# Optimization experiments

Measured on AMD Instinct MI355X. Metric: run time of the kernel, lower is better.

## Reference

```python
import jax, jax.numpy as jnp
import numpy as np

DIM = 2048
N_HEADS = 32
N_KV_HEADS = 8
HEAD_DIM = DIM // N_HEADS  # 64
SEQ = 2048
BATCH = 2


def _rope_freqs(seq_len, head_dim, theta=10000.0):
    inv = 1.0 / (theta ** (np.arange(0, head_dim, 2)[: head_dim // 2].astype(np.float32) / head_dim))
    t = np.arange(seq_len, dtype=np.float32)
    ang = np.outer(t, inv)  # (seq, head_dim//2)
    return jnp.asarray(np.cos(ang)), jnp.asarray(np.sin(ang))


def setup_inputs() -> dict:
    key = jax.random.key(0)
    ks = jax.random.split(key, 5)
    x = jax.random.normal(ks[0], (BATCH, SEQ, DIM), dtype=jnp.float32)
    s = 1.0 / np.sqrt(DIM)
    wq = jax.random.normal(ks[1], (N_HEADS * HEAD_DIM, DIM), dtype=jnp.float32) * s
    wk = jax.random.normal(ks[2], (N_KV_HEADS * HEAD_DIM, DIM), dtype=jnp.float32) * s
    wv = jax.random.normal(ks[3], (N_KV_HEADS * HEAD_DIM, DIM), dtype=jnp.float32) * s
    wo = jax.random.normal(ks[4], (DIM, N_HEADS * HEAD_DIM), dtype=jnp.float32) * s
    freqs_cos, freqs_sin = _rope_freqs(SEQ, HEAD_DIM)
    return {"x": x, "freqs_cos": freqs_cos, "freqs_sin": freqs_sin,
            "wq": wq, "wk": wk, "wv": wv, "wo": wo}


def _apply_rope(t, cos, sin):
    # t: (B, S, H, D); cos/sin: (S, D//2) broadcast to (1, S, 1, D//2)
    B, S, H, D = t.shape
    tr = t.reshape(B, S, H, D // 2, 2)
    x0, x1 = tr[..., 0], tr[..., 1]
    c = cos[None, :, None, :]
    s = sin[None, :, None, :]
    o0 = x0 * c - x1 * s
    o1 = x0 * s + x1 * c
    return jnp.stack([o0, o1], axis=-1).reshape(B, S, H, D)


def reference(x, freqs_cos, freqs_sin, wq, wk, wv, wo):
    B, S, _ = x.shape
    H, KV, D = N_HEADS, N_KV_HEADS, HEAD_DIM
    rep = H // KV
    xq = jnp.einsum('bsd,hd->bsh', x, wq).reshape(B, S, H, D)
    xk = jnp.einsum('bsd,hd->bsh', x, wk).reshape(B, S, KV, D)
    xv = jnp.einsum('bsd,hd->bsh', x, wv).reshape(B, S, KV, D)
    xq = _apply_rope(xq, freqs_cos, freqs_sin)
    xk = _apply_rope(xk, freqs_cos, freqs_sin)
    # GQA without materializing repeated K/V: group q heads as (KV, rep).
    # repeat_interleave on dim=2 maps q head h -> kv head h // rep.
    xqg = xq.reshape(B, S, KV, rep, D)
    scale = 1.0 / jnp.sqrt(jnp.float32(D))
    scores = jnp.einsum('bqkrd,bskd->bkrqs', xqg, xk) * scale  # (B,KV,rep,S,S)
    causal = jnp.tril(jnp.ones((S, S), dtype=bool))
    scores = jnp.where(causal[None, None, None], scores, jnp.float32(-jnp.inf))
    probs = jax.nn.softmax(scores, axis=-1)
    out = jnp.einsum('bkrqs,bskd->bqkrd', probs, xv)  # (B,S,KV,rep,D)
    out = out.reshape(B, S, H * D)
    return jnp.einsum('bsh,dh->bsd', out, wo)
```

## Files before the change

kernel.cpp:

```cpp
#include <hip/hip_runtime.h>

#define DIMSZ 2048
#define NH 32
#define NKV 8
#define HD 64
#define SEQLEN 2048
#define BATCH 2
#define NROWS (BATCH*SEQLEN)
#define NQKVC 3072

typedef __bf16 bf16x8 __attribute__((ext_vector_type(8)));
typedef __bf16 bf16x2 __attribute__((ext_vector_type(2)));
typedef float f32x4v __attribute__((ext_vector_type(4)));
typedef float f32x2v __attribute__((ext_vector_type(2)));
typedef float f32x16 __attribute__((ext_vector_type(16)));

__device__ __forceinline__ unsigned short f2bf(float f) {
  __bf16 h = (__bf16)f;
  union { __bf16 h; unsigned short u; } v; v.h = h; return v.u;
}
__device__ __forceinline__ unsigned int pk2bf(float lo, float hi) {
  f32x2v v; v[0] = lo; v[1] = hi;
  bf16x2 h = __builtin_convertvector(v, bf16x2);
  union { bf16x2 h; unsigned int u; } c; c.h = h; return c.u;
}
__device__ __forceinline__ int swz128(int row, int colBytes) {
  return row * 128 + (colBytes ^ ((row & 7) << 4));
}

#define GLOAD16(g, l) __builtin_amdgcn_global_load_lds( \
    (const __attribute__((address_space(1))) unsigned int*)(g), \
    (__attribute__((address_space(3))) unsigned int*)(l), 16, 0, 0)

__global__ void k_cvt_all(const float* __restrict__ x,
                          const float* __restrict__ wq, const float* __restrict__ wk,
                          const float* __restrict__ wv, const float* __restrict__ wo,
                          unsigned short* __restrict__ xb,
                          unsigned short* __restrict__ wqkvb,
                          unsigned short* __restrict__ wob) {
  int i = blockIdx.x * 256 + threadIdx.x;
  const float* s; unsigned short* d; int soff, doff;
  if (i < 2097152)        { s = x;  d = xb;    soff = i;           doff = i; }
  else if (i < 3145728)   { s = wq; d = wqkvb; soff = i - 2097152; doff = i - 2097152; }
  else if (i < 3407872)   { s = wk; d = wqkvb; soff = i - 3145728; doff = i - 2097152; }
  else if (i < 3670016)   { s = wv; d = wqkvb; soff = i - 3407872; doff = i - 2097152; }
  else                    { s = wo; d = wob;   soff = i - 3670016; doff = i - 3670016; }
  float4 v = reinterpret_cast<const float4*>(s)[soff];
  uint2 pk; pk.x = pk2bf(v.x, v.y); pk.y = pk2bf(v.z, v.w);
  reinterpret_cast<uint2*>(d)[doff] = pk;
}

__global__ __launch_bounds__(256, 2) void k_gemm_qkv(
    const unsigned short* __restrict__ A,
    const unsigned short* __restrict__ B,
    const float* __restrict__ fc, const float* __restrict__ fs,
    unsigned short* __restrict__ Qb, unsigned short* __restrict__ Kb,
    unsigned short* __restrict__ Vt)
{
  constexpr int BK = 64, K = DIMSZ;
  __shared__ __attribute__((aligned(16))) unsigned short smA[128 * BK];
  __shared__ __attribute__((aligned(16))) unsigned short smB[128 * BK];
  const int tid = threadIdx.x;
  const int lane = tid & 63;
  const int wid = tid >> 6;
  const int lr = lane & 15, lg = lane >> 4;
  const int gx = gridDim.x;
  int lin = blockIdx.y * gx + blockIdx.x;
  const int cpx = (gx * gridDim.y) >> 3;
  lin = (lin & 7) * cpx + (lin >> 3);
  const int m0 = (lin / gx) * 128, n0 = (lin % gx) * 128;
  const int wr = (wid >> 1) * 64, wc = (wid & 1) * 64;

  f32x4v acc[4][4];
  #pragma unroll
  for (int i = 0; i < 4; i++)
    #pragma unroll
    for (int j = 0; j < 4; j++)
      acc[i][j] = f32x4v{0.f, 0.f, 0.f, 0.f};

  for (int k0 = 0; k0 < K; k0 += BK) {
    #pragma unroll
    for (int c = 0; c < 4; c++) {
      const int chunk = wid * 4 + c;
      const int idx = chunk * 64 + lane;
      const int row = idx >> 3, s = idx & 7;
      const int ks = (s ^ (row & 7)) * 8;
      GLOAD16(A + (size_t)(m0 + row) * K + k0 + ks, &smA[chunk * 512]);
      GLOAD16(B + (size_t)(n0 + row) * K + k0 + ks, &smB[chunk * 512]);
    }
    __syncthreads();
    #pragma unroll
    for (int ks = 0; ks < 2; ks++) {
      bf16x8 af[4], bfv[4];
      #pragma unroll
      for (int m = 0; m < 4; m++)
        af[m] = *reinterpret_cast<const bf16x8*>((char*)smA + swz128(wr + m * 16 + lr, ks * 64 + lg * 16));
      #pragma unroll
      for (int n = 0; n < 4; n++)
        bfv[n] = *reinterpret_cast<const bf16x8*>((char*)smB + swz128(wc + n * 16 + lr, ks * 64 + lg * 16));
      #pragma unroll
      for (int m = 0; m < 4; m++)
        #pragma unroll
        for (int n = 0; n < 4; n++)
          acc[m][n] = __builtin_amdgcn_mfma_f32_16x16x32_bf16(af[m], bfv[n], acc[m][n], 0, 0, 0);
    }
    __syncthreads();
  }
  const int bx = n0 >> 7;
  if (bx < 20) {
    const bool isQ = bx < 16;
    const float SCL = isQ ? 0.18033688011112043f : 1.0f;
    #pragma unroll
    for (int n = 0; n < 4; n++) {
      const int col = n0 + wc + n * 16 + lr;
      const int d = col & 63;
      const int i = d >> 1;
      const float sgn = (d & 1) ? 1.0f : -1.0f;
      unsigned short* dst;
      if (isQ) dst = Qb + (size_t)(col >> 6) * (SEQLEN * HD) + d;
      else     dst = Kb + (size_t)((col - 2048) >> 6) * (SEQLEN * HD) + d;
      #pragma unroll
      for (int m = 0; m < 4; m++)
        #pragma unroll
        for (int r = 0; r < 4; r++) {
          const int row = m0 + wr + m * 16 + lg * 4 + r;
          const int s = row & (SEQLEN - 1), b = row >> 11;
          const float v = acc[m][n][r];
          const float p = __shfl_xor(v, 1);
          const float c = fc[s * 32 + i], sn = fs[s * 32 + i];
          const float o = (v * c + sgn * p * sn) * SCL;
          const size_t headStride = (size_t)(isQ ? NH : NKV) * SEQLEN * HD;
          dst[(size_t)b * headStride + (size_t)s * HD] = f2bf(o);
        }
    }
  } else {
    #pragma unroll
    for (int n = 0; n < 4; n++) {
      const int col = n0 + wc + n * 16 + lr;
      const int kvh = (col - 2560) >> 6, d = col & 63;
      #pragma unroll
      for (int m = 0; m < 4; m++) {
        const int row0 = m0 + wr + m * 16 + lg * 4;
        const int s0 = row0 & (SEQLEN - 1), b = row0 >> 11;
        uint2 pk;
        pk.x = pk2bf(acc[m][n][0], acc[m][n][1]);
        pk.y = pk2bf(acc[m][n][2], acc[m][n][3]);
        *reinterpret_cast<uint2*>(
            Vt + ((size_t)((b * NKV + kvh) * HD) + d) * SEQLEN + s0) = pk;
      }
    }
  }
}

template<int OUT_BF16>
__global__ __launch_bounds__(256, 2) void k_gemm_bt(
    const unsigned short* __restrict__ A,
    const unsigned short* __restrict__ B,
    void* __restrict__ Cv, int M, int N, int K)
{
  constexpr int BK = 64;
  __shared__ __attribute__((aligned(16))) unsigned short smA[128 * BK];
  __shared__ __attribute__((aligned(16))) unsigned short smB[128 * BK];
  const int tid = threadIdx.x;
  const int lane = tid & 63;
  const int wid = tid >> 6;
  const int lr = lane & 15, lg = lane >> 4;
  const int gx = gridDim.x;
  int lin = blockIdx.y * gx + blockIdx.x;
  const int cpx = (gx * gridDim.y) >> 3;
  lin = (lin & 7) * cpx + (lin >> 3);
  const int m0 = (lin / gx) * 128, n0 = (lin % gx) * 128;
  const int wr = (wid >> 1) * 64, wc = (wid & 1) * 64;

  f32x4v acc[4][4];
  #pragma unroll
  for (int i = 0; i < 4; i++)
    #pragma unroll
    for (int j = 0; j < 4; j++)
      acc[i][j] = f32x4v{0.f, 0.f, 0.f, 0.f};

  for (int k0 = 0; k0 < K; k0 += BK) {
    #pragma unroll
    for (int c = 0; c < 4; c++) {
      const int chunk = wid * 4 + c;
      const int idx = chunk * 64 + lane;
      const int row = idx >> 3, s = idx & 7;
      const int ks = (s ^ (row & 7)) * 8;
      GLOAD16(A + (size_t)(m0 + row) * K + k0 + ks, &smA[chunk * 512]);
      GLOAD16(B + (size_t)(n0 + row) * K + k0 + ks, &smB[chunk * 512]);
    }
    __syncthreads();
    #pragma unroll
    for (int ks = 0; ks < 2; ks++) {
      bf16x8 af[4], bfv[4];
      #pragma unroll
      for (int m = 0; m < 4; m++)
        af[m] = *reinterpret_cast<const bf16x8*>((char*)smA + swz128(wr + m * 16 + lr, ks * 64 + lg * 16));
      #pragma unroll
      for (int n = 0; n < 4; n++)
        bfv[n] = *reinterpret_cast<const bf16x8*>((char*)smB + swz128(wc + n * 16 + lr, ks * 64 + lg * 16));
      #pragma unroll
      for (int m = 0; m < 4; m++)
        #pragma unroll
        for (int n = 0; n < 4; n++)
          acc[m][n] = __builtin_amdgcn_mfma_f32_16x16x32_bf16(af[m], bfv[n], acc[m][n], 0, 0, 0);
    }
    __syncthreads();
  }
  #pragma unroll
  for (int m = 0; m < 4; m++)
    #pragma unroll
    for (int n = 0; n < 4; n++)
      #pragma unroll
      for (int r = 0; r < 4; r++) {
        const size_t row = m0 + wr + m * 16 + lg * 4 + r;
        const size_t col = n0 + wc + n * 16 + lr;
        if (OUT_BF16) ((unsigned short*)Cv)[row * N + col] = f2bf(acc[m][n][r]);
        else          ((float*)Cv)[row * N + col] = acc[m][n][r];
      }
}

__global__ __launch_bounds__(256, 2) void k_attn(
    const unsigned short* __restrict__ Qg,
    const unsigned short* __restrict__ Kg,
    const unsigned short* __restrict__ Vt,
    unsigned short* __restrict__ Og)
{
  constexpr int KVB = 64;
  __shared__ __attribute__((aligned(16))) unsigned short sK0[KVB * HD];
  __shared__ __attribute__((aligned(16))) unsigned short sK1[KVB * HD];
  __shared__ __attribute__((aligned(16))) unsigned short sV0[HD * KVB];
  __shared__ __attribute__((aligned(16))) unsigned short sV1[HD * KVB];
  const int tid = threadIdx.x;
  const int lane = tid & 63, wid = tid >> 6;
  const int l31 = lane & 31, hi = lane >> 5;
  const int orig = blockIdx.x;
  const int w = (orig & 7) * 64 + (orig >> 3);
  const int kvh = w >> 6;
  const int b = (w >> 5) & 1;
  const int h = kvh * 4 + ((w >> 3) & 3);
  const int qp = w & 7;
  const unsigned short* Qp = Qg + ((size_t)(b * NH + h) * SEQLEN) * HD;
  const unsigned short* Kp = Kg + ((size_t)(b * NKV + kvh) * SEQLEN) * HD;
  const unsigned short* Vp = Vt + ((size_t)(b * NKV + kvh) * HD) * SEQLEN;

  int srow[2], scol[2];
  #pragma unroll
  for (int cc = 0; cc < 2; cc++) {
    const int idx = (wid * 2 + cc) * 64 + lane;
    srow[cc] = idx >> 3;
    scol[cc] = ((idx & 7) ^ (srow[cc] & 7)) * 8;
  }

  for (int phase = 0; phase < 2; phase++) {
    const int qt = phase ? (15 - qp) : qp;
    const int qrow0 = qt * 128 + wid * 32;
    const int qg = qrow0 + l31;
    bf16x8 aq[4];
    #pragma unroll
    for (int ks = 0; ks < 4; ks++)
      aq[ks] = *reinterpret_cast<const bf16x8*>(Qp + (size_t)qg * HD + ks * 16 + hi * 8);

    f32x16 accO0, accO1;
    #pragma unroll
    for (int ii = 0; ii < 16; ii++) { accO0[ii] = 0.f; accO1[ii] = 0.f; }
    float mrun = -3.0e38f, lrun = 0.f;

    auto STAGE_K = [&](int t, unsigned short* buf) {
      #pragma unroll
      for (int cc = 0; cc < 2; cc++)
        GLOAD16(Kp + (size_t)(t * KVB + srow[cc]) * HD + scol[cc], &buf[(wid * 2 + cc) * 512]);
    };
    auto STAGE_V = [&](int t, unsigned short* buf) {
      #pragma unroll
      for (int cc = 0; cc < 2; cc++)
        GLOAD16(Vp + (size_t)srow[cc] * SEQLEN + t * KVB + scol[cc], &buf[(wid * 2 + cc) * 512]);
    };
    auto QK = [&](int kv0, const unsigned short* bK, f32x16& S0, f32x16& S1) {
      if (kv0 > qrow0 + 31) return;
      #pragma unroll
      for (int ii = 0; ii < 16; ii++) { S0[ii] = 0.f; S1[ii] = 0.f; }
      __builtin_amdgcn_s_setprio(1);
      #pragma unroll
      for (int ks = 0; ks < 4; ks++) {
        bf16x8 ak0 = *reinterpret_cast<const bf16x8*>((const char*)bK + swz128(l31,      ks * 32 + hi * 16));
        bf16x8 ak1 = *reinterpret_cast<const bf16x8*>((const char*)bK + swz128(32 + l31, ks * 32 + hi * 16));
        S0 = __builtin_amdgcn_mfma_f32_32x32x16_bf16(ak0, aq[ks], S0, 0, 0, 0);
        S1 = __builtin_amdgcn_mfma_f32_32x32x16_bf16(ak1, aq[ks], S1, 0, 0, 0);
      }
      __builtin_amdgcn_s_setprio(0);
    };
    auto SMPV = [&](int kv0, const unsigned short* bV, f32x16& S0, f32x16& S1) {
      if (kv0 > qrow0 + 31) return;
      if (kv0 + KVB - 1 > qrow0) {
        #pragma unroll
        for (int reg = 0; reg < 16; reg++) {
          const int rl = (reg & 3) + 8 * (reg >> 2) + (hi << 2);
          if (kv0 + rl > qg)      S0[reg] = -1.0e30f;
          if (kv0 + 32 + rl > qg) S1[reg] = -1.0e30f;
        }
      }
      float t16[16];
      #pragma unroll
      for (int ii = 0; ii < 16; ii++) t16[ii] = fmaxf(S0[ii], S1[ii]);
      float t8[8];
      #pragma unroll
      for (int ii = 0; ii < 8; ii++) t8[ii] = fmaxf(t16[ii], t16[ii + 8]);
      float t4[4];
      #pragma unroll
      for (int ii = 0; ii < 4; ii++) t4[ii] = fmaxf(t8[ii], t8[ii + 4]);
      float tm = fmaxf(fmaxf(t4[0], t4[1]), fmaxf(t4[2], t4[3]));
      tm = fmaxf(tm, __shfl_xor(tm, 32));
      const float mo = mrun;
      const bool defer = __all(tm <= mo + 8.0f);
      const float mn = defer ? mo : fmaxf(mo, tm);
      #pragma unroll
      for (int ii = 0; ii < 16; ii++) {
        S0[ii] = __builtin_amdgcn_exp2f(S0[ii] - mn);
        S1[ii] = __builtin_amdgcn_exp2f(S1[ii] - mn);
      }
      float u16[16];
      #pragma unroll
      for (int ii = 0; ii < 16; ii++) u16[ii] = S0[ii] + S1[ii];
      float u8[8];
      #pragma unroll
      for (int ii = 0; ii < 8; ii++) u8[ii] = u16[ii] + u16[ii + 8];
      float u4[4];
      #pragma unroll
      for (int ii = 0; ii < 4; ii++) u4[ii] = u8[ii] + u8[ii + 4];
      float rs = (u4[0] + u4[1]) + (u4[2] + u4[3]);
      rs += __shfl_xor(rs, 32);
      if (defer) {
        lrun += rs;
      } else {
        const float sc = __builtin_amdgcn_exp2f(mo - mn);
        mrun = mn;
        lrun = lrun * sc + rs;
        #pragma unroll
        for (int reg = 0; reg < 16; reg++) {
          const int rl = (reg & 3) + 8 * (reg >> 2) + (hi << 2);
          const float scr = __shfl(sc, rl);
          accO0[reg] *= scr; accO1[reg] *= scr;
        }
      }
      __builtin_amdgcn_s_setprio(1);
      #define PVSTEP(S16, G, CB) do {                                          \
        unsigned a0 = pk2bf(S16[(G)+0], S16[(G)+1]);                           \
        unsigned a1 = pk2bf(S16[(G)+2], S16[(G)+3]);                           \
        unsigned b0 = pk2bf(S16[(G)+4], S16[(G)+5]);                           \
        unsigned b1 = pk2bf(S16[(G)+6], S16[(G)+7]);                           \
        unsigned s0 = hi ? a0 : b0, s1 = hi ? a1 : b1;                         \
        unsigned r0 = __shfl_xor((int)s0, 32), r1 = __shfl_xor((int)s1, 32);   \
        union { unsigned u[4]; bf16x8 v; } pf;                                 \
        pf.u[0] = hi ? r0 : a0; pf.u[1] = hi ? r1 : a1;                        \
        pf.u[2] = hi ? b0 : r0; pf.u[3] = hi ? b1 : r1;                        \
        bf16x8 bv0 = *reinterpret_cast<const bf16x8*>((const char*)bV + swz128(l31,      (CB))); \
        bf16x8 bv1 = *reinterpret_cast<const bf16x8*>((const char*)bV + swz128(32 + l31, (CB))); \
        accO0 = __builtin_amdgcn_mfma_f32_32x32x16_bf16(pf.v, bv0, accO0, 0, 0, 0); \
        accO1 = __builtin_amdgcn_mfma_f32_32x32x16_bf16(pf.v, bv1, accO1, 0, 0, 0); \
      } while (0)
      PVSTEP(S0, 0,  0  + hi * 16);
      PVSTEP(S0, 8,  32 + hi * 16);
      PVSTEP(S1, 0,  64 + hi * 16);
      PVSTEP(S1, 8,  96 + hi * 16);
      #undef PVSTEP
      __builtin_amdgcn_s_setprio(0);
    };

    const int nt = qt * 2 + 2;
    f32x16 Sa0, Sa1, Sb0, Sb1;
    STAGE_K(0, sK0);
    STAGE_V(0, sV0);
    __syncthreads();
    STAGE_K(1, sK1);
    QK(0, sK0, Sa0, Sa1);
    for (int t = 0; t < nt; t += 2) {
      __syncthreads();
      if (t + 2 < nt) STAGE_K(t + 2, sK0);
      STAGE_V(t + 1, sV1);
      QK((t + 1) * KVB, sK1, Sb0, Sb1);
      SMPV(t * KVB, sV0, Sa0, Sa1);
      __syncthreads();
      if (t + 3 < nt) STAGE_K(t + 3, sK1);
      if (t + 2 < nt) { STAGE_V(t + 2, sV0); QK((t + 2) * KVB, sK0, Sa0, Sa1); }
      SMPV((t + 1) * KVB, sV1, Sb0, Sb1);
    }
    const float inv = 1.0f / lrun;
    #pragma unroll
    for (int reg = 0; reg < 16; reg++) {
      const int rl = (reg & 3) + 8 * (reg >> 2) + (hi << 2);
      const float invr = __shfl(inv, rl);
      const int q = qrow0 + rl;
      const size_t base = ((size_t)(b * SEQLEN + q)) * DIMSZ + h * HD;
      Og[base + l31]      = f2bf(accO0[reg] * invr);
      Og[base + 32 + l31] = f2bf(accO1[reg] * invr);
    }
  }
}

extern "C" void kernel_launch(void* const* d_in, const int* in_sizes, int n_in,
                              void* d_out, int out_size, void* d_ws, size_t ws_size,
                              hipStream_t stream)
{
  const float* x  = (const float*)d_in[0];
  const float* fc = (const float*)d_in[1];
  const float* fs = (const float*)d_in[2];
  const float* wq = (const float*)d_in[3];
  const float* wk = (const float*)d_in[4];
  const float* wv = (const float*)d_in[5];
  const float* wo = (const float*)d_in[6];
  float* out = (float*)d_out;
  char* ws = (char*)d_ws;

  unsigned short* xb    = (unsigned short*)(ws + 0);
  unsigned short* wqkvb = (unsigned short*)(ws + 16777216);
  unsigned short* wob   = (unsigned short*)(ws + 29360128);
  unsigned short* Qb    = (unsigned short*)(ws + 62914560);
  unsigned short* Kb    = (unsigned short*)(ws + 79691776);
  unsigned short* Vtb   = (unsigned short*)(ws + 83886080);
  unsigned short* attnb = (unsigned short*)(ws + 88080384);

  k_cvt_all<<<18432, 256, 0, stream>>>(x, wq, wk, wv, wo, xb, wqkvb, wob);

  dim3 g1(24, 32);
  k_gemm_qkv<<<g1, 256, 0, stream>>>(xb, wqkvb, fc, fs, Qb, Kb, Vtb);

  k_attn<<<512, 256, 0, stream>>>(Qb, Kb, Vtb, attnb);

  dim3 g2(16, 32);
  k_gemm_bt<0><<<g2, 256, 0, stream>>>(attnb, wob, out, NROWS, DIMSZ, DIMSZ);
}
```

Measured before the change: 171.4 us.

## Process KV tiles in pairs with four-deep LDS buffering in attention

```diff
diff --git a/kernel.cpp b/kernel.cpp
--- a/kernel.cpp
+++ b/kernel.cpp
@@ -229,8 +229,12 @@
   constexpr int KVB = 64;
   __shared__ __attribute__((aligned(16))) unsigned short sK0[KVB * HD];
   __shared__ __attribute__((aligned(16))) unsigned short sK1[KVB * HD];
+  __shared__ __attribute__((aligned(16))) unsigned short sK2[KVB * HD];
+  __shared__ __attribute__((aligned(16))) unsigned short sK3[KVB * HD];
   __shared__ __attribute__((aligned(16))) unsigned short sV0[HD * KVB];
   __shared__ __attribute__((aligned(16))) unsigned short sV1[HD * KVB];
+  __shared__ __attribute__((aligned(16))) unsigned short sV2[HD * KVB];
+  __shared__ __attribute__((aligned(16))) unsigned short sV3[HD * KVB];
   const int tid = threadIdx.x;
   const int lane = tid & 63, wid = tid >> 6;
   const int l31 = lane & 31, hi = lane >> 5;
@@ -276,33 +280,40 @@
       for (int cc = 0; cc < 2; cc++)
         GLOAD16(Vp + (size_t)srow[cc] * SEQLEN + t * KVB + scol[cc], &buf[(wid * 2 + cc) * 512]);
     };
-    auto QK = [&](int kv0, const unsigned short* bK, f32x16& S0, f32x16& S1) {
+
+    auto PAIR = [&](int kv0, const unsigned short* bKa, const unsigned short* bKb,
+                    const unsigned short* bVa, const unsigned short* bVb) {
       if (kv0 > qrow0 + 31) return;
-      #pragma unroll
-      for (int ii = 0; ii < 16; ii++) { S0[ii] = 0.f; S1[ii] = 0.f; }
+      f32x16 SA0, SA1, SB0, SB1;
+      #pragma unroll
+      for (int ii = 0; ii < 16; ii++) { SA0[ii] = 0.f; SA1[ii] = 0.f; SB0[ii] = 0.f; SB1[ii] = 0.f; }
       __builtin_amdgcn_s_setprio(1);
       #pragma unroll
       for (int ks = 0; ks < 4; ks++) {
-        bf16x8 ak0 = *reinterpret_cast<const bf16x8*>((const char*)bK + swz128(l31,      ks * 32 + hi * 16));
-        bf16x8 ak1 = *reinterpret_cast<const bf16x8*>((const char*)bK + swz128(32 + l31, ks * 32 + hi * 16));
-        S0 = __builtin_amdgcn_mfma_f32_32x32x16_bf16(ak0, aq[ks], S0, 0, 0, 0);
-        S1 = __builtin_amdgcn_mfma_f32_32x32x16_bf16(ak1, aq[ks], S1, 0, 0, 0);
+        bf16x8 a0 = *reinterpret_cast<const bf16x8*>((const char*)bKa + swz128(l31,      ks * 32 + hi * 16));
+        bf16x8 a1 = *reinterpret_cast<const bf16x8*>((const char*)bKa + swz128(32 + l31, ks * 32 + hi * 16));
+        bf16x8 b0 = *reinterpret_cast<const bf16x8*>((const char*)bKb + swz128(l31,      ks * 32 + hi * 16));
+        bf16x8 b1 = *reinterpret_cast<const bf16x8*>((const char*)bKb + swz128(32 + l31, ks * 32 + hi * 16));
+        SA0 = __builtin_amdgcn_mfma_f32_32x32x16_bf16(a0, aq[ks], SA0, 0, 0, 0);
+        SA1 = __builtin_amdgcn_mfma_f32_32x32x16_bf16(a1, aq[ks], SA1, 0, 0, 0);
+        SB0 = __builtin_amdgcn_mfma_f32_32x32x16_bf16(b0, aq[ks], SB0, 0, 0, 0);
+        SB1 = __builtin_amdgcn_mfma_f32_32x32x16_bf16(b1, aq[ks], SB1, 0, 0, 0);
       }
       __builtin_amdgcn_s_setprio(0);
-    };
-    auto SMPV = [&](int kv0, const unsigned short* bV, f32x16& S0, f32x16& S1) {
-      if (kv0 > qrow0 + 31) return;
-      if (kv0 + KVB - 1 > qrow0) {
+      if (kv0 + 2 * KVB - 1 > qrow0) {
         #pragma unroll
         for (int reg = 0; reg < 16; reg++) {
           const int rl = (reg & 3) + 8 * (reg >> 2) + (hi << 2);
-          if (kv0 + rl > qg)      S0[reg] = -1.0e30f;
-          if (kv0 + 32 + rl > qg) S1[reg] = -1.0e30f;
+          if (kv0 + rl > qg)      SA0[reg] = -1.0e30f;
+          if (kv0 + 32 + rl > qg) SA1[reg] = -1.0e30f;
+          if (kv0 + 64 + rl > qg) SB0[reg] = -1.0e30f;
+          if (kv0 + 96 + rl > qg) SB1[reg] = -1.0e30f;
         }
       }
       float t16[16];
       #pragma unroll
-      for (int ii = 0; ii < 16; ii++) t16[ii] = fmaxf(S0[ii], S1[ii]);
+      for (int ii = 0; ii < 16; ii++)
+        t16[ii] = fmaxf(fmaxf(SA0[ii], SA1[ii]), fmaxf(SB0[ii], SB1[ii]));
       float t8[8];
       #pragma unroll
       for (int ii = 0; ii < 8; ii++) t8[ii] = fmaxf(t16[ii], t16[ii + 8]);
@@ -316,12 +327,15 @@
       const float mn = defer ? mo : fmaxf(mo, tm);
       #pragma unroll
       for (int ii = 0; ii < 16; ii++) {
-        S0[ii] = __builtin_amdgcn_exp2f(S0[ii] - mn);
-        S1[ii] = __builtin_amdgcn_exp2f(S1[ii] - mn);
+        SA0[ii] = __builtin_amdgcn_exp2f(SA0[ii] - mn);
+        SA1[ii] = __builtin_amdgcn_exp2f(SA1[ii] - mn);
+        SB0[ii] = __builtin_amdgcn_exp2f(SB0[ii] - mn);
+        SB1[ii] = __builtin_amdgcn_exp2f(SB1[ii] - mn);
       }
       float u16[16];
       #pragma unroll
-      for (int ii = 0; ii < 16; ii++) u16[ii] = S0[ii] + S1[ii];
+      for (int ii = 0; ii < 16; ii++)
+        u16[ii] = (SA0[ii] + SA1[ii]) + (SB0[ii] + SB1[ii]);
       float u8[8];
       #pragma unroll
       for (int ii = 0; ii < 8; ii++) u8[ii] = u16[ii] + u16[ii + 8];
@@ -344,7 +358,7 @@
         }
       }
       __builtin_amdgcn_s_setprio(1);
-      #define PVSTEP(S16, G, CB) do {                                          \
+      #define PVSTEP(S16, G, BV, CB) do {                                      \
         unsigned a0 = pk2bf(S16[(G)+0], S16[(G)+1]);                           \
         unsigned a1 = pk2bf(S16[(G)+2], S16[(G)+3]);                           \
         unsigned b0 = pk2bf(S16[(G)+4], S16[(G)+5]);                           \
@@ -354,36 +368,38 @@
         union { unsigned u[4]; bf16x8 v; } pf;                                 \
         pf.u[0] = hi ? r0 : a0; pf.u[1] = hi ? r1 : a1;                        \
         pf.u[2] = hi ? b0 : r0; pf.u[3] = hi ? b1 : r1;                        \
-        bf16x8 bv0 = *reinterpret_cast<const bf16x8*>((const char*)bV + swz128(l31,      (CB))); \
-        bf16x8 bv1 = *reinterpret_cast<const bf16x8*>((const char*)bV + swz128(32 + l31, (CB))); \
+        bf16x8 bv0 = *reinterpret_cast<const bf16x8*>((const char*)(BV) + swz128(l31,      (CB))); \
+        bf16x8 bv1 = *reinterpret_cast<const bf16x8*>((const char*)(BV) + swz128(32 + l31, (CB))); \
         accO0 = __builtin_amdgcn_mfma_f32_32x32x16_bf16(pf.v, bv0, accO0, 0, 0, 0); \
         accO1 = __builtin_amdgcn_mfma_f32_32x32x16_bf16(pf.v, bv1, accO1, 0, 0, 0); \
       } while (0)
-      PVSTEP(S0, 0,  0  + hi * 16);
-      PVSTEP(S0, 8,  32 + hi * 16);
-      PVSTEP(S1, 0,  64 + hi * 16);
-      PVSTEP(S1, 8,  96 + hi * 16);
+      PVSTEP(SA0, 0, bVa,  0  + hi * 16);
+      PVSTEP(SA0, 8, bVa,  32 + hi * 16);
+      PVSTEP(SA1, 0, bVa,  64 + hi * 16);
+      PVSTEP(SA1, 8, bVa,  96 + hi * 16);
+      PVSTEP(SB0, 0, bVb,  0  + hi * 16);
+      PVSTEP(SB0, 8, bVb,  32 + hi * 16);
+      PVSTEP(SB1, 0, bVb,  64 + hi * 16);
+      PVSTEP(SB1, 8, bVb,  96 + hi * 16);
       #undef PVSTEP
       __builtin_amdgcn_s_setprio(0);
     };
 
     const int nt = qt * 2 + 2;
-    f32x16 Sa0, Sa1, Sb0, Sb1;
-    STAGE_K(0, sK0);
-    STAGE_V(0, sV0);
+    STAGE_K(0, sK0); STAGE_K(1, sK1);
+    STAGE_V(0, sV0); STAGE_V(1, sV1);
     __syncthreads();
-    STAGE_K(1, sK1);
-    QK(0, sK0, Sa0, Sa1);
-    for (int t = 0; t < nt; t += 2) {
+    for (int t = 0; t < nt; t += 4) {
+      if (t + 2 < nt) { STAGE_K(t + 2, sK2); STAGE_K(t + 3, sK3);
+                        STAGE_V(t + 2, sV2); STAGE_V(t + 3, sV3); }
+      PAIR(t * KVB, sK0, sK1, sV0, sV1);
       __syncthreads();
-      if (t + 2 < nt) STAGE_K(t + 2, sK0);
-      STAGE_V(t + 1, sV1);
-      QK((t + 1) * KVB, sK1, Sb0, Sb1);
-      SMPV(t * KVB, sV0, Sa0, Sa1);
-      __syncthreads();
-      if (t + 3 < nt) STAGE_K(t + 3, sK1);
-      if (t + 2 < nt) { STAGE_V(t + 2, sV0); QK((t + 2) * KVB, sK0, Sa0, Sa1); }
-      SMPV((t + 1) * KVB, sV1, Sb0, Sb1);
+      if (t + 2 < nt) {
+        if (t + 4 < nt) { STAGE_K(t + 4, sK0); STAGE_K(t + 5, sK1);
+                          STAGE_V(t + 4, sV0); STAGE_V(t + 5, sV1); }
+        PAIR((t + 2) * KVB, sK2, sK3, sV2, sV3);
+        __syncthreads();
+      }
     }
     const float inv = 1.0f / lrun;
     #pragma unroll
```

Measured after the change: 171.8 us. No clear change (+0.3%).

## Split attention KV loop across two wave groups with final softmax merge

Applied to the files above, without the earlier changes.

```diff
diff --git a/kernel.cpp b/kernel.cpp
--- a/kernel.cpp
+++ b/kernel.cpp
@@ -220,19 +220,19 @@
       }
 }
 
-__global__ __launch_bounds__(256, 2) void k_attn(
+__global__ __launch_bounds__(512, 2) void k_attn(
     const unsigned short* __restrict__ Qg,
     const unsigned short* __restrict__ Kg,
     const unsigned short* __restrict__ Vt,
     unsigned short* __restrict__ Og)
 {
   constexpr int KVB = 64;
-  __shared__ __attribute__((aligned(16))) unsigned short sK0[KVB * HD];
-  __shared__ __attribute__((aligned(16))) unsigned short sK1[KVB * HD];
-  __shared__ __attribute__((aligned(16))) unsigned short sV0[HD * KVB];
-  __shared__ __attribute__((aligned(16))) unsigned short sV1[HD * KVB];
+  __shared__ __attribute__((aligned(16))) unsigned short smem[32768];
+  constexpr int KA0 = 0, KA1 = 4096, KB0 = 8192, KB1 = 12288;
+  constexpr int VA0 = 16384, VA1 = 20480, VB0 = 24576, VB1 = 28672;
   const int tid = threadIdx.x;
   const int lane = tid & 63, wid = tid >> 6;
+  const int group = wid >> 2;
   const int l31 = lane & 31, hi = lane >> 5;
   const int orig = blockIdx.x;
   const int w = (orig & 7) * 64 + (orig >> 3);
@@ -244,17 +244,13 @@
   const unsigned short* Kp = Kg + ((size_t)(b * NKV + kvh) * SEQLEN) * HD;
   const unsigned short* Vp = Vt + ((size_t)(b * NKV + kvh) * HD) * SEQLEN;
 
-  int srow[2], scol[2];
-  #pragma unroll
-  for (int cc = 0; cc < 2; cc++) {
-    const int idx = (wid * 2 + cc) * 64 + lane;
-    srow[cc] = idx >> 3;
-    scol[cc] = ((idx & 7) ^ (srow[cc] & 7)) * 8;
-  }
+  const int sidx = wid * 64 + lane;
+  const int srow = sidx >> 3;
+  const int scol = ((sidx & 7) ^ (srow & 7)) * 8;
 
   for (int phase = 0; phase < 2; phase++) {
     const int qt = phase ? (15 - qp) : qp;
-    const int qrow0 = qt * 128 + wid * 32;
+    const int qrow0 = qt * 128 + (wid & 3) * 32;
     const int qg = qrow0 + l31;
     bf16x8 aq[4];
     #pragma unroll
@@ -266,18 +262,13 @@
     for (int ii = 0; ii < 16; ii++) { accO0[ii] = 0.f; accO1[ii] = 0.f; }
     float mrun = -3.0e38f, lrun = 0.f;
 
-    auto STAGE_K = [&](int t, unsigned short* buf) {
-      #pragma unroll
-      for (int cc = 0; cc < 2; cc++)
-        GLOAD16(Kp + (size_t)(t * KVB + srow[cc]) * HD + scol[cc], &buf[(wid * 2 + cc) * 512]);
+    auto STAGE_K = [&](int t, int off) {
+      GLOAD16(Kp + (size_t)(t * KVB + srow) * HD + scol, &smem[off + wid * 512]);
     };
-    auto STAGE_V = [&](int t, unsigned short* buf) {
-      #pragma unroll
-      for (int cc = 0; cc < 2; cc++)
-        GLOAD16(Vp + (size_t)srow[cc] * SEQLEN + t * KVB + scol[cc], &buf[(wid * 2 + cc) * 512]);
+    auto STAGE_V = [&](int t, int off) {
+      GLOAD16(Vp + (size_t)srow * SEQLEN + t * KVB + scol, &smem[off + wid * 512]);
     };
     auto QK = [&](int kv0, const unsigned short* bK, f32x16& S0, f32x16& S1) {
-      if (kv0 > qrow0 + 31) return;
       #pragma unroll
       for (int ii = 0; ii < 16; ii++) { S0[ii] = 0.f; S1[ii] = 0.f; }
       __builtin_amdgcn_s_setprio(1);
@@ -291,7 +282,6 @@
       __builtin_amdgcn_s_setprio(0);
     };
     auto SMPV = [&](int kv0, const unsigned short* bV, f32x16& S0, f32x16& S1) {
-      if (kv0 > qrow0 + 31) return;
       if (kv0 + KVB - 1 > qrow0) {
         #pragma unroll
         for (int reg = 0; reg < 16; reg++) {
@@ -366,35 +356,75 @@
       #undef PVSTEP
       __builtin_amdgcn_s_setprio(0);
     };
+    auto GSTEP = [&](int tb, int kOff0, int vOff0, int kOff1, int vOff1) {
+      if (group == 0) {
+        const int kv0 = tb * KVB;
+        if (kv0 <= qrow0 + 31) {
+          f32x16 S0, S1;
+          QK(kv0, &smem[kOff0], S0, S1);
+          SMPV(kv0, &smem[vOff0], S0, S1);
+        }
+      } else {
+        const int kv0 = (tb + 1) * KVB;
+        if (kv0 <= qrow0 + 31) {
+          f32x16 S0, S1;
+          QK(kv0, &smem[kOff1], S0, S1);
+          SMPV(kv0, &smem[vOff1], S0, S1);
+        }
+      }
+    };
 
     const int nt = qt * 2 + 2;
-    f32x16 Sa0, Sa1, Sb0, Sb1;
-    STAGE_K(0, sK0);
-    STAGE_V(0, sV0);
-    __syncthreads();
-    STAGE_K(1, sK1);
-    QK(0, sK0, Sa0, Sa1);
-    for (int t = 0; t < nt; t += 2) {
+    STAGE_K(0, KA0); STAGE_K(1, KA1);
+    STAGE_V(0, VA0); STAGE_V(1, VA1);
+    __syncthreads();
+    for (int t = 0; t < nt; t += 4) {
+      if (t + 2 < nt) { STAGE_K(t + 2, KB0); STAGE_K(t + 3, KB1);
+                        STAGE_V(t + 2, VB0); STAGE_V(t + 3, VB1); }
+      GSTEP(t, KA0, VA0, KA1, VA1);
       __syncthreads();
-      if (t + 2 < nt) STAGE_K(t + 2, sK0);
-      STAGE_V(t + 1, sV1);
-      QK((t + 1) * KVB, sK1, Sb0, Sb1);
-      SMPV(t * KVB, sV0, Sa0, Sa1);
-      __syncthreads();
-      if (t + 3 < nt) STAGE_K(t + 3, sK1);
-      if (t + 2 < nt) { STAGE_V(t + 2, sV0); QK((t + 2) * KVB, sK0, Sa0, Sa1); }
-      SMPV((t + 1) * KVB, sV1, Sb0, Sb1);
-    }
-    const float inv = 1.0f / lrun;
-    #pragma unroll
-    for (int reg = 0; reg < 16; reg++) {
-      const int rl = (reg & 3) + 8 * (reg >> 2) + (hi << 2);
-      const float invr = __shfl(inv, rl);
-      const int q = qrow0 + rl;
-      const size_t base = ((size_t)(b * SEQLEN + q)) * DIMSZ + h * HD;
-      Og[base + l31]      = f2bf(accO0[reg] * invr);
-      Og[base + 32 + l31] = f2bf(accO1[reg] * invr);
-    }
+      if (t + 2 < nt) {
+        if (t + 4 < nt) { STAGE_K(t + 4, KA0); STAGE_K(t + 5, KA1);
+                          STAGE_V(t + 4, VA0); STAGE_V(t + 5, VA1); }
+        GSTEP(t + 2, KB0, VB0, KB1, VB1);
+        __syncthreads();
+      }
+    }
+    float* mO  = (float*)smem;
+    float* mML = (float*)(smem + 16384);
+    if (wid >= 4) {
+      const int w4 = wid - 4;
+      #pragma unroll
+      for (int reg = 0; reg < 16; reg++) {
+        mO[((w4 * 32 + reg) * 64) + lane]      = accO0[reg];
+        mO[((w4 * 32 + 16 + reg) * 64) + lane] = accO1[reg];
+      }
+      mML[(w4 * 64 + lane) * 2 + 0] = mrun;
+      mML[(w4 * 64 + lane) * 2 + 1] = lrun;
+    }
+    __syncthreads();
+    if (wid < 4) {
+      const float m1 = mML[(wid * 64 + lane) * 2 + 0];
+      const float l1 = mML[(wid * 64 + lane) * 2 + 1];
+      const float ms = fmaxf(mrun, m1);
+      const float c0 = __builtin_amdgcn_exp2f(mrun - ms);
+      const float c1 = __builtin_amdgcn_exp2f(m1 - ms);
+      const float inv = 1.0f / (lrun * c0 + l1 * c1);
+      #pragma unroll
+      for (int reg = 0; reg < 16; reg++) {
+        const int rl = (reg & 3) + 8 * (reg >> 2) + (hi << 2);
+        const float c0r = __shfl(c0, rl);
+        const float c1r = __shfl(c1, rl);
+        const float invr = __shfl(inv, rl);
+        const float o1a = mO[((wid * 32 + reg) * 64) + lane];
+        const float o1b = mO[((wid * 32 + 16 + reg) * 64) + lane];
+        const int q = qrow0 + rl;
+        const size_t base = ((size_t)(b * SEQLEN + q)) * DIMSZ + h * HD;
+        Og[base + l31]      = f2bf((accO0[reg] * c0r + o1a * c1r) * invr);
+        Og[base + 32 + l31] = f2bf((accO1[reg] * c0r + o1b * c1r) * invr);
+      }
+    }
+    __syncthreads();
   }
 }
 
@@ -425,7 +455,7 @@
   dim3 g1(24, 32);
   k_gemm_qkv<<<g1, 256, 0, stream>>>(xb, wqkvb, fc, fs, Qb, Kb, Vtb);
 
-  k_attn<<<512, 256, 0, stream>>>(Qb, Kb, Vtb, attnb);
+  k_attn<<<512, 512, 0, stream>>>(Qb, Kb, Vtb, attnb);
 
   dim3 g2(16, 32);
   k_gemm_bt<0><<<g2, 256, 0, stream>>>(attnb, wob, out, NROWS, DIMSZ, DIMSZ);
```

Result: slower. 180.0 us (+5.1%).
